# Kernel tuning notes

Measured on AMD Instinct MI355X. Metric: run time of the kernel, lower is better.

Reference implementation:

```python
import jax, jax.numpy as jnp
import numpy as np
from jax import lax

N_VAR, BATCH, N_IN, N_OUT, N_FEAT, T = 4, 32, 32, 32, 32, 256
EPS, COUPLING, GMAX, GMIN = 0.05, 0.2, 10.0, 0.01
DT, RMIN, RMAX, CMIN, CMAX = 0.1, 1e5, 1e7, 1e-7, 1e-4
ETA = np.array([0.05, 0.5, 0.3, 3.0], dtype=np.float32)  # printed-tanh activation params


def _init_theta(key, n_in, n_out):
    # xavier_uniform -> min-max normalize to [0,1], then bias-column construction as in pLayer.__init__
    a = float(np.sqrt(6.0 / (n_in + 2 + n_out)))
    t = jax.random.uniform(key, (n_in + 2, n_out), minval=-a, maxval=a)
    t = (t - t.min()) / (t.max() - t.min())
    t = t.at[-1, :].add(GMAX)
    t = t.at[-2, :].set(ETA[2] / (1.0 - ETA[2]) * (t[:-2].sum(0) + t[-1]))
    return t.astype(jnp.float32)


def setup_inputs():
    key = jax.random.key(0)
    kx, k1, k2 = jax.random.split(key, 3)
    x = jax.random.uniform(kx, (N_VAR, BATCH, N_IN, T), dtype=jnp.float32)
    theta1_ = _init_theta(k1, N_IN, N_OUT)
    theta2_ = _init_theta(k2, N_OUT * (N_FEAT + 1), N_OUT)
    # LearnableFilter init from beta_init (C_ fixed at -10, R_ is logit of normalized R)
    betas = np.linspace(0.1, 0.9, N_OUT)
    b0 = betas[:N_FEAT]
    b1 = betas[::-1][:N_FEAT]
    C_mean = 1.0 / (1.0 + np.exp(10.0)) * (CMAX - CMIN) + CMIN
    def r_(b):
        R_true = b * DT / (1.0 - b) / C_mean
        Rn = (R_true - RMIN) / (RMAX - RMIN)
        return np.log(Rn / (1.0 - Rn))
    Rlf_ = jnp.asarray(np.broadcast_to(np.stack([r_(b0), r_(b1)], -1), (N_OUT, N_FEAT, 2)).copy(), dtype=jnp.float32)
    Clf_ = jnp.full((N_OUT, N_FEAT, 2), -10.0, dtype=jnp.float32)
    return {"x": x, "theta1_": theta1_, "theta2_": theta2_, "Rlf_": Rlf_, "Clf_": Clf_}


def _theta_eff(theta_):
    # clamp + magnitude pruning with straight-through estimator
    t = jnp.clip(theta_, -GMAX, GMAX)
    t = jnp.where(jnp.abs(t) < GMIN, 0.0, t)
    return lax.stop_gradient(t) + theta_ - lax.stop_gradient(theta_)


def _pmac(a, theta_, key):
    # a: [N,B,Cin,T] -> [N,B,Cout,T]; printed MAC with sign-split weights and ideal inverter INV(a)=-a
    th = _theta_eff(theta_)
    noise = (jax.random.uniform(key, (N_VAR,) + th.shape) * 2.0 - 1.0) * EPS + 1.0
    thn = th[None] * noise  # [N,M,O]
    W = jnp.abs(thn) / (jnp.sum(jnp.abs(thn), axis=1, keepdims=True) + 1e-10)
    pos = (thn >= 0).astype(a.dtype)
    neg = 1.0 - pos
    ar = jnp.swapaxes(a, 2, 3)  # [N,B,T,Cin]
    ones = jnp.ones(ar.shape[:-1] + (1,), a.dtype)
    a_ext = jnp.concatenate([ar, ones, jnp.zeros_like(ones)], axis=-1)  # [N,B,T,M]
    a_neg = (-a_ext).at[..., -1].set(0.0)  # INV(a_ext) with last column zeroed
    z = jnp.einsum('nbtm,nmo->nbto', a_ext, W * pos) + jnp.einsum('nbtm,nmo->nbto', a_neg, W * neg)
    act = ETA[0] + ETA[1] * jnp.tanh((z - ETA[2]) * ETA[3])
    return jnp.swapaxes(act, 2, 3)


def _filter_bank(x, R_, C_, key):
    # x: [K,N,B,T]; first-order leaky integrator with fresh per-step R/C/mu noise, random init state
    K, N, B, Tt = x.shape
    Rt = jax.nn.sigmoid(R_) * (RMAX - RMIN) + RMIN  # [K]
    Ct = jax.nn.sigmoid(C_) * (CMAX - CMIN) + CMIN
    kR, kC, kmu, k0 = jax.random.split(key, 4)
    nR = (jax.random.uniform(kR, (Tt, K, N, 1)) * 2.0 - 1.0) * EPS + 1.0
    nC = (jax.random.uniform(kC, (Tt, K, N, 1)) * 2.0 - 1.0) * EPS + 1.0
    mu = jax.random.uniform(kmu, (Tt, K, N, 1)) * COUPLING + 1.0
    RC = mu * (Rt[None, :, None, None] * nR) * (Ct[None, :, None, None] * nC)
    beta = RC / (RC + DT)  # [T,K,N,1]
    s0 = jax.random.uniform(k0, (K, N, B))  # random_state=True
    xs = jnp.moveaxis(x, 3, 0)  # [T,K,N,B]
    def step(s, inp):
        x_t, b_t = inp
        return b_t * s + (1.0 - b_t) * x_t, s  # emit pre-update state (torch keeps init, drops last)
    _, outs = lax.scan(step, s0, (xs, beta))
    return jnp.moveaxis(outs, 0, 3)  # [K,N,B,T]


def reference(x, theta1_, theta2_, Rlf_, Clf_):
    key = jax.random.key(42)
    k1, k2, k3, k4 = jax.random.split(key, 4)
    a1 = _pmac(x, theta1_, k1)  # [N,B,C,T]
    N, B, C, Tt = a1.shape
    F = N_FEAT
    K = C * F
    xc = jnp.transpose(a1, (2, 0, 1, 3))  # [C,N,B,T]
    xk = jnp.broadcast_to(xc[:, None], (C, F, N, B, Tt)).reshape(K, N, B, Tt)
    y = _filter_bank(xk, Rlf_[..., 0].reshape(K), Clf_[..., 0].reshape(K), k2)
    y = _filter_bank(y, Rlf_[..., 1].reshape(K), Clf_[..., 1].reshape(K), k3)
    y = y.reshape(C, F, N, B, Tt)
    feats = jnp.concatenate([xc[:, None], y], axis=1)  # [C,F+1,N,B,T]
    h = jnp.transpose(feats, (2, 3, 0, 1, 4)).reshape(N, B, C * (F + 1), Tt)
    return _pmac(h, theta2_, k4)  # [N,B,N_out,T]
```

## Files before the change

### kernel.cpp

```cpp
#include <hip/hip_runtime.h>
#include <stdint.h>

#define C_RMIN 100000.0f
#define C_RMAX 10000000.0f
#define C_CMIN 1e-07f
#define C_CMAX 1e-04f
#define C_DT   0.1f
#define C_EPS  0.05f
#define C_COUP 0.2f

typedef __attribute__((ext_vector_type(8))) short bf16x8;
typedef __attribute__((ext_vector_type(4))) float floatx4;

__host__ __device__ inline void tf2x32(uint32_t k0, uint32_t k1,
                                       uint32_t& x0, uint32_t& x1) {
  uint32_t ks2 = k0 ^ k1 ^ 0x1BD11BDAu;
  uint32_t a = x0 + k0, b = x1 + k1;
#define TFR(r) a += b; b = (b << (r)) | (b >> (32 - (r))); b ^= a;
  TFR(13) TFR(15) TFR(26) TFR(6)
  a += k1;  b += ks2 + 1u;
  TFR(17) TFR(29) TFR(16) TFR(24)
  a += ks2; b += k0 + 2u;
  TFR(13) TFR(15) TFR(26) TFR(6)
  a += k0;  b += k1 + 3u;
  TFR(17) TFR(29) TFR(16) TFR(24)
  a += k1;  b += ks2 + 4u;
  TFR(13) TFR(15) TFR(26) TFR(6)
  a += ks2; b += k0 + 5u;
#undef TFR
  x0 = a; x1 = b;
}

__device__ inline float unif01(uint32_t k0, uint32_t k1, uint32_t e) {
  uint32_t x0 = 0u, x1 = e;
  tf2x32(k0, k1, x0, x1);
  uint32_t bits = x0 ^ x1;
  return __uint_as_float((bits >> 9) | 0x3F800000u) - 1.0f;
}

__device__ inline float theta_eff(float t) {
  t = fminf(fmaxf(t, -10.0f), 10.0f);
  return (fabsf(t) < 0.01f) ? 0.0f : t;
}

__device__ inline float sigmoidf(float x) { return 1.0f / (1.0f + expf(-x)); }

__device__ inline float noise_mul(float u) { return (u * 2.0f - 1.0f) * C_EPS + 1.0f; }

__global__ __launch_bounds__(256) void prep0_kernel(
    const float* __restrict__ Rlf, const float* __restrict__ Clf,
    const float* __restrict__ theta1, const float* __restrict__ theta2,
    float* __restrict__ beta12, float* __restrict__ S1eff,
    float* __restrict__ denom2p,
    uint32_t k1a, uint32_t k1b, uint32_t k4a, uint32_t k4b,
    uint32_t kR1a, uint32_t kR1b, uint32_t kC1a, uint32_t kC1b,
    uint32_t kM1a, uint32_t kM1b,
    uint32_t kR2a, uint32_t kR2b, uint32_t kC2a, uint32_t kC2b,
    uint32_t kM2a, uint32_t kM2b) {
  int bid = blockIdx.x;
  if (bid < 32) {
    int n = bid >> 3, p = bid & 7;
    int o = threadIdx.x & 31;
    int jc = threadIdx.x >> 5;
    int j0 = p * 8 + jc;
    float part = 0.0f;
    for (int j = j0; j < 1058; j += 64) {
      float t = theta_eff(theta2[j * 32 + o]);
      float u = unif01(k4a, k4b, (uint32_t)((n * 1058 + j) * 32 + o));
      part += fabsf(t * noise_mul(u));
    }
    __shared__ float red[256];
    red[jc * 32 + o] = part;
    __syncthreads();
    if (jc == 0) {
      float s = 0.0f;
      for (int q = 0; q < 8; ++q) s += red[q * 32 + o];
      denom2p[(n * 8 + p) * 32 + o] = s;
    }
  } else if (bid < 36) {
    int n = bid - 32;
    int o = threadIdx.x;
    if (o < 32) {
      float tn[34];
      float den = 0.0f;
      for (int m = 0; m < 34; ++m) {
        float t = theta_eff(theta1[m * 32 + o]);
        float u = unif01(k1a, k1b, (uint32_t)((n * 34 + m) * 32 + o));
        float v = t * noise_mul(u);
        tn[m] = v;
        den += fabsf(v);
      }
      den += 1e-10f;
      for (int m = 0; m < 33; ++m)
        S1eff[(n * 33 + m) * 32 + o] = tn[m] / den;
    }
  } else {
    int u = (bid - 36) * 256 + threadIdx.x;
    int k = u & 1023;
    int tc = (u >> 10) & 31;
    int n = u >> 15;
    float Rt1 = sigmoidf(Rlf[k * 2 + 0]) * (C_RMAX - C_RMIN) + C_RMIN;
    float Ct1 = sigmoidf(Clf[k * 2 + 0]) * (C_CMAX - C_CMIN) + C_CMIN;
    float Rt2 = sigmoidf(Rlf[k * 2 + 1]) * (C_RMAX - C_RMIN) + C_RMIN;
    float Ct2 = sigmoidf(Clf[k * 2 + 1]) * (C_CMAX - C_CMIN) + C_CMIN;
#pragma unroll
    for (int it = 0; it < 8; ++it) {
      int t = tc * 8 + it;
      uint32_t e = (uint32_t)((t * 1024 + k) * 4 + n);
      float nR1 = noise_mul(unif01(kR1a, kR1b, e));
      float nC1 = noise_mul(unif01(kC1a, kC1b, e));
      float mu1 = unif01(kM1a, kM1b, e) * C_COUP + 1.0f;
      float rc1 = mu1 * (Rt1 * nR1) * (Ct1 * nC1);
      float nR2 = noise_mul(unif01(kR2a, kR2b, e));
      float nC2 = noise_mul(unif01(kC2a, kC2b, e));
      float mu2 = unif01(kM2a, kM2b, e) * C_COUP + 1.0f;
      float rc2 = mu2 * (Rt2 * nR2) * (Ct2 * nC2);
      float2 bb = { rc1 / (rc1 + C_DT), rc2 / (rc2 + C_DT) };
      *(float2*)&beta12[(size_t)(((n * 256 + t) * 1024) + k) * 2] = bb;
    }
  }
}

__global__ __launch_bounds__(256) void prep1_kernel(
    const float* __restrict__ theta2, const float* __restrict__ denom2p,
    float* __restrict__ S2eff,
    const float* __restrict__ x, const float* __restrict__ S1eff,
    float* __restrict__ a1, uint32_t k4a, uint32_t k4b) {
  int bid = blockIdx.x;
  __shared__ float xs[32][256];
  if (bid < 128) {
    int n = bid >> 5, b = bid & 31;
    int t = threadIdx.x;
    const float* xp = x + (size_t)((n * 32 + b) * 32) * 256;
    for (int m = 0; m < 32; ++m) xs[m][t] = xp[m * 256 + t];
    __syncthreads();
    const float* S = S1eff + n * 33 * 32;
    float* ap = a1 + (size_t)((n * 32 + b) * 32) * 256;
    for (int o = 0; o < 32; ++o) {
      float z = S[32 * 32 + o];
#pragma unroll
      for (int m = 0; m < 32; ++m) z += xs[m][t] * S[m * 32 + o];
      ap[o * 256 + t] = 0.05f + 0.5f * tanhf((z - 0.3f) * 3.0f);
    }
  } else {
    int idx = (bid - 128) * 256 + threadIdx.x;
    if (idx >= 4 * 1057 * 32) return;
    int o = idx & 31;
    int r = idx >> 5;
    int j = r % 1057;
    int n = r / 1057;
    float den = 1e-10f;
#pragma unroll
    for (int p = 0; p < 8; ++p) den += denom2p[(n * 8 + p) * 32 + o];
    float t = theta_eff(theta2[j * 32 + o]);
    float u = unif01(k4a, k4b, (uint32_t)((n * 1058 + j) * 32 + o));
    S2eff[idx] = t * noise_mul(u) / den;
  }
}

#define YP 264
#define YPLANE (16 * YP)

__global__ __launch_bounds__(320) void fk5_kernel(
    const float* __restrict__ a1, const float* __restrict__ S2eff,
    const float* __restrict__ beta12, float* __restrict__ zpart,
    uint32_t k01a, uint32_t k01b, uint32_t k02a, uint32_t k02b) {
  int bid = blockIdx.x;
  int qr = bid & 3;
  int nb = bid >> 2;
  int n = nb >> 5, b = nb & 31;
  int tid = threadIdx.x;

  __shared__ __align__(16) uint8_t smem[50176];
  uint16_t* yh = (uint16_t*)smem;
  uint16_t* yl = (uint16_t*)(smem + 16896);
  short*    wf = (short*)(smem + 33792);

  const float* S2n = S2eff + (size_t)n * 1057 * 32;
  const float* a1nb = a1 + (size_t)nb * 8192;
  const float* bp = beta12 + ((size_t)n * 262144 + qr * 256) * 2;
  float* zout = zpart + (size_t)bid * 8192;

  float s1 = 0.0f, s2 = 0.0f;
  int cc = 0;

  if (tid < 256) {
    int k = qr * 256 + tid;
    uint32_t e0 = (uint32_t)((k * 4 + n) * 32 + b);
    s1 = unif01(k01a, k01b, e0);
    s2 = unif01(k02a, k02b, e0);
    cc = k >> 5;
    for (int it = 0; it < 32; ++it) {
      int widx = it * 256 + tid;
      int j = widx & 7;
      int lane_ = (widx >> 3) & 63;
      int ot = (widx >> 9) & 1;
      int ks = widx >> 10;
      int sub = ((lane_ >> 4) << 3) + j;
      int jrow = (qr * 8 + ks) * 33 + 1 + sub;
      float w = S2n[jrow * 32 + ot * 16 + (lane_ & 15)];
      uint32_t wb = __float_as_uint(w);
      uint32_t hi = (wb + 0x7FFFu + ((wb >> 16) & 1u)) >> 16;
      wf[(ks * 2 + ot) * 512 + lane_ * 8 + j] = (short)(uint16_t)hi;
    }
  }
  __syncthreads();

  for (int c = 0; c <= 16; ++c) {
    if (tid < 256) {
      if (c < 16) {
        uint16_t* yhb = yh + (c & 1) * YPLANE;
        uint16_t* ylb = yl + (c & 1) * YPLANE;
        int t0 = c * 16;
#pragma unroll
        for (int it = 0; it < 16; ++it) {
          int t = t0 + it;
          uint32_t sb = __float_as_uint(s2);
          uint32_t hi = sb >> 16;
          float fhi = __uint_as_float(sb & 0xFFFF0000u);
          uint32_t lo = __float_as_uint(s2 - fhi) >> 16;
          yhb[it * YP + tid] = (uint16_t)hi;
          ylb[it * YP + tid] = (uint16_t)lo;
          float2 bb = *(const float2*)&bp[(size_t)(t * 1024 + tid) * 2];
          float xv = a1nb[cc * 256 + t];
          s2 = bb.y * s2 + (1.0f - bb.y) * s1;
          s1 = bb.x * s1 + (1.0f - bb.x) * xv;
        }
      }
    } else if (c >= 1) {
      int lane = tid - 256;
      int tc = lane & 15, q = lane >> 4;
      const uint16_t* yhr = yh + ((c - 1) & 1) * YPLANE + tc * YP + q * 8;
      const uint16_t* ylr = yl + ((c - 1) & 1) * YPLANE + tc * YP + q * 8;
      floatx4 acc0a = {0,0,0,0}, acc0b = {0,0,0,0};
      floatx4 acc1a = {0,0,0,0}, acc1b = {0,0,0,0};
#pragma unroll
      for (int ks = 0; ks < 8; ++ks) {
        bf16x8 ah = *(const bf16x8*)(yhr + ks * 32);
        bf16x8 al = *(const bf16x8*)(ylr + ks * 32);
        bf16x8 bh0 = *(const bf16x8*)&wf[(ks * 2 + 0) * 512 + lane * 8];
        bf16x8 bh1 = *(const bf16x8*)&wf[(ks * 2 + 1) * 512 + lane * 8];
        if (ks & 1) {
          acc0b = __builtin_amdgcn_mfma_f32_16x16x32_bf16(ah, bh0, acc0b, 0, 0, 0);
          acc0b = __builtin_amdgcn_mfma_f32_16x16x32_bf16(al, bh0, acc0b, 0, 0, 0);
          acc1b = __builtin_amdgcn_mfma_f32_16x16x32_bf16(ah, bh1, acc1b, 0, 0, 0);
          acc1b = __builtin_amdgcn_mfma_f32_16x16x32_bf16(al, bh1, acc1b, 0, 0, 0);
        } else {
          acc0a = __builtin_amdgcn_mfma_f32_16x16x32_bf16(ah, bh0, acc0a, 0, 0, 0);
          acc0a = __builtin_amdgcn_mfma_f32_16x16x32_bf16(al, bh0, acc0a, 0, 0, 0);
          acc1a = __builtin_amdgcn_mfma_f32_16x16x32_bf16(ah, bh1, acc1a, 0, 0, 0);
          acc1a = __builtin_amdgcn_mfma_f32_16x16x32_bf16(al, bh1, acc1a, 0, 0, 0);
        }
      }
      int t0 = (c - 1) * 16;
      floatx4 r0 = acc0a + acc0b;
      floatx4 r1 = acc1a + acc1b;
      *(floatx4*)&zout[tc * 256 + t0 + q * 4] = r0;
      *(floatx4*)&zout[(16 + tc) * 256 + t0 + q * 4] = r1;
    }
    __syncthreads();
  }
}

__global__ __launch_bounds__(256) void cb_kernel(
    const float* __restrict__ a1, const float* __restrict__ S2eff,
    const float* __restrict__ zpart, float* __restrict__ out) {
  int nb = blockIdx.x;
  int n = nb >> 5;
  int t = threadIdx.x;
  __shared__ float xs[32][256];
  const float* a1nb = a1 + (size_t)nb * 8192;
  for (int c = 0; c < 32; ++c) xs[c][t] = a1nb[c * 256 + t];
  __syncthreads();
  const float* S2n = S2eff + (size_t)n * 1057 * 32;
  const float* zp = zpart + (size_t)nb * 4 * 8192;
  float* op = out + (size_t)nb * 8192;
  for (int o = 0; o < 32; ++o) {
    float z = S2n[1056 * 32 + o];
#pragma unroll
    for (int c = 0; c < 32; ++c) z += xs[c][t] * S2n[(c * 33) * 32 + o];
    z += zp[o * 256 + t] + zp[8192 + o * 256 + t] +
         zp[16384 + o * 256 + t] + zp[24576 + o * 256 + t];
    op[o * 256 + t] = 0.05f + 0.5f * tanhf((z - 0.3f) * 3.0f);
  }
}

struct KeyPair { uint32_t a, b; };

static inline void split4_host(KeyPair key, KeyPair out[4]) {
  for (uint32_t i = 0; i < 4; ++i) {
    uint32_t x0 = 0u, x1 = i;
    tf2x32(key.a, key.b, x0, x1);
    out[i] = {x0, x1};
  }
}

extern "C" void kernel_launch(void* const* d_in, const int* in_sizes, int n_in,
                              void* d_out, int out_size, void* d_ws, size_t ws_size,
                              hipStream_t stream) {
  const float* x   = (const float*)d_in[0];
  const float* th1 = (const float*)d_in[1];
  const float* th2 = (const float*)d_in[2];
  const float* Rlf = (const float*)d_in[3];
  const float* Clf = (const float*)d_in[4];
  float* out = (float*)d_out;
  float* ws = (float*)d_ws;

  float* S1     = ws;
  float* den2p  = ws + 4224;
  float* S2     = ws + 5248;
  float* a1     = ws + 140544;
  float* beta12 = ws + 1189120;
  float* zpart  = ws + 3286272;

  KeyPair root{0u, 42u};
  KeyPair kk[4];  split4_host(root, kk);
  KeyPair f1[4];  split4_host(kk[1], f1);
  KeyPair f2[4];  split4_host(kk[2], f2);

  prep0_kernel<<<dim3(548), dim3(256), 0, stream>>>(
      Rlf, Clf, th1, th2, beta12, S1, den2p,
      kk[0].a, kk[0].b, kk[3].a, kk[3].b,
      f1[0].a, f1[0].b, f1[1].a, f1[1].b, f1[2].a, f1[2].b,
      f2[0].a, f2[0].b, f2[1].a, f2[1].b, f2[2].a, f2[2].b);
  prep1_kernel<<<dim3(657), dim3(256), 0, stream>>>(
      th2, den2p, S2, x, S1, a1, kk[3].a, kk[3].b);
  fk5_kernel<<<dim3(512), dim3(320), 0, stream>>>(
      a1, S2, beta12, zpart, f1[3].a, f1[3].b, f2[3].a, f2[3].b);
  cb_kernel<<<dim3(128), dim3(256), 0, stream>>>(a1, S2, zpart, out);
}
```

Before: 158.7 us.

## Fuse prep kernels and compute second-layer weights on the fly in consumers

Removes the separate prep1 kernel by computing the first-layer weights inside each layer-1 MAC block and generating the second-layer normalized noisy weights directly in fk6 and cb2 from theta2 and the partial denominators. This drops one kernel launch and the S1/S2 global round trips. In exchange, the threefry noise and the layer-1 normalization are recomputed redundantly per block, and the layer-1 MAC now competes with beta generation inside one kernel.

Result: faster. 142.8 us (-10.1%).

```diff
diff --git a/kernel.cpp b/kernel.cpp
--- a/kernel.cpp
+++ b/kernel.cpp
@@ -47,21 +47,27 @@
 
 __device__ inline float noise_mul(float u) { return (u * 2.0f - 1.0f) * C_EPS + 1.0f; }
 
-__global__ __launch_bounds__(256) void prep0_kernel(
+__global__ __launch_bounds__(256) void prep_kernel(
     const float* __restrict__ Rlf, const float* __restrict__ Clf,
     const float* __restrict__ theta1, const float* __restrict__ theta2,
-    float* __restrict__ beta12, float* __restrict__ S1eff,
+    const float* __restrict__ x,
+    float* __restrict__ beta12, float* __restrict__ a1,
     float* __restrict__ denom2p,
     uint32_t k1a, uint32_t k1b, uint32_t k4a, uint32_t k4b,
     uint32_t kR1a, uint32_t kR1b, uint32_t kC1a, uint32_t kC1b,
     uint32_t kM1a, uint32_t kM1b,
     uint32_t kR2a, uint32_t kR2b, uint32_t kC2a, uint32_t kC2b,
     uint32_t kM2a, uint32_t kM2b) {
+  __shared__ float red[256];
+  __shared__ float vsm[34 * 32];
+  __shared__ float S1s[33 * 32];
+  __shared__ float xs[32][256];
   int bid = blockIdx.x;
+  int tid = threadIdx.x;
   if (bid < 32) {
     int n = bid >> 3, p = bid & 7;
-    int o = threadIdx.x & 31;
-    int jc = threadIdx.x >> 5;
+    int o = tid & 31;
+    int jc = tid >> 5;
     int j0 = p * 8 + jc;
     float part = 0.0f;
     for (int j = j0; j < 1058; j += 64) {
@@ -69,7 +75,6 @@
       float u = unif01(k4a, k4b, (uint32_t)((n * 1058 + j) * 32 + o));
       part += fabsf(t * noise_mul(u));
     }
-    __shared__ float red[256];
     red[jc * 32 + o] = part;
     __syncthreads();
     if (jc == 0) {
@@ -77,25 +82,39 @@
       for (int q = 0; q < 8; ++q) s += red[q * 32 + o];
       denom2p[(n * 8 + p) * 32 + o] = s;
     }
-  } else if (bid < 36) {
-    int n = bid - 32;
-    int o = threadIdx.x;
-    if (o < 32) {
-      float tn[34];
-      float den = 0.0f;
-      for (int m = 0; m < 34; ++m) {
-        float t = theta_eff(theta1[m * 32 + o]);
-        float u = unif01(k1a, k1b, (uint32_t)((n * 34 + m) * 32 + o));
-        float v = t * noise_mul(u);
-        tn[m] = v;
-        den += fabsf(v);
-      }
-      den += 1e-10f;
-      for (int m = 0; m < 33; ++m)
-        S1eff[(n * 33 + m) * 32 + o] = tn[m] / den;
+  } else if (bid < 160) {
+    int blk = bid - 32;
+    int n = blk >> 5, b = blk & 31;
+    int o = tid & 31, mq = tid >> 5;
+    float dp = 0.0f;
+    for (int m = mq; m < 34; m += 8) {
+      float t = theta_eff(theta1[m * 32 + o]);
+      float v = t * noise_mul(unif01(k1a, k1b, (uint32_t)((n * 34 + m) * 32 + o)));
+      vsm[m * 32 + o] = v;
+      dp += fabsf(v);
+    }
+    red[mq * 32 + o] = dp;
+    const float* xp = x + (size_t)((n * 32 + b) * 32) * 256;
+    __syncthreads();
+    for (int idx = tid; idx < 33 * 32; idx += 256) {
+      int oo = idx & 31;
+      float den = 1e-10f;
+#pragma unroll
+      for (int q = 0; q < 8; ++q) den += red[q * 32 + oo];
+      S1s[idx] = vsm[idx] / den;
+    }
+    for (int m = 0; m < 32; ++m) xs[m][tid] = xp[m * 256 + tid];
+    __syncthreads();
+    float* ap = a1 + (size_t)((n * 32 + b) * 32) * 256;
+    int t = tid;
+    for (int oo = 0; oo < 32; ++oo) {
+      float z = S1s[32 * 32 + oo];
+#pragma unroll
+      for (int m = 0; m < 32; ++m) z += xs[m][t] * S1s[m * 32 + oo];
+      ap[oo * 256 + t] = 0.05f + 0.5f * tanhf((z - 0.3f) * 3.0f);
     }
   } else {
-    int u = (bid - 36) * 256 + threadIdx.x;
+    int u = (bid - 160) * 256 + tid;
     int k = u & 1023;
     int tc = (u >> 10) & 31;
     int n = u >> 15;
@@ -121,50 +140,15 @@
   }
 }
 
-__global__ __launch_bounds__(256) void prep1_kernel(
-    const float* __restrict__ theta2, const float* __restrict__ denom2p,
-    float* __restrict__ S2eff,
-    const float* __restrict__ x, const float* __restrict__ S1eff,
-    float* __restrict__ a1, uint32_t k4a, uint32_t k4b) {
-  int bid = blockIdx.x;
-  __shared__ float xs[32][256];
-  if (bid < 128) {
-    int n = bid >> 5, b = bid & 31;
-    int t = threadIdx.x;
-    const float* xp = x + (size_t)((n * 32 + b) * 32) * 256;
-    for (int m = 0; m < 32; ++m) xs[m][t] = xp[m * 256 + t];
-    __syncthreads();
-    const float* S = S1eff + n * 33 * 32;
-    float* ap = a1 + (size_t)((n * 32 + b) * 32) * 256;
-    for (int o = 0; o < 32; ++o) {
-      float z = S[32 * 32 + o];
-#pragma unroll
-      for (int m = 0; m < 32; ++m) z += xs[m][t] * S[m * 32 + o];
-      ap[o * 256 + t] = 0.05f + 0.5f * tanhf((z - 0.3f) * 3.0f);
-    }
-  } else {
-    int idx = (bid - 128) * 256 + threadIdx.x;
-    if (idx >= 4 * 1057 * 32) return;
-    int o = idx & 31;
-    int r = idx >> 5;
-    int j = r % 1057;
-    int n = r / 1057;
-    float den = 1e-10f;
-#pragma unroll
-    for (int p = 0; p < 8; ++p) den += denom2p[(n * 8 + p) * 32 + o];
-    float t = theta_eff(theta2[j * 32 + o]);
-    float u = unif01(k4a, k4b, (uint32_t)((n * 1058 + j) * 32 + o));
-    S2eff[idx] = t * noise_mul(u) / den;
-  }
-}
-
 #define YP 264
 #define YPLANE (16 * YP)
 
-__global__ __launch_bounds__(320) void fk5_kernel(
-    const float* __restrict__ a1, const float* __restrict__ S2eff,
+__global__ __launch_bounds__(320) void fk6_kernel(
+    const float* __restrict__ a1, const float* __restrict__ theta2,
+    const float* __restrict__ denom2p,
     const float* __restrict__ beta12, float* __restrict__ zpart,
-    uint32_t k01a, uint32_t k01b, uint32_t k02a, uint32_t k02b) {
+    uint32_t k01a, uint32_t k01b, uint32_t k02a, uint32_t k02b,
+    uint32_t k4a, uint32_t k4b) {
   int bid = blockIdx.x;
   int qr = bid & 3;
   int nb = bid >> 2;
@@ -175,11 +159,19 @@
   uint16_t* yh = (uint16_t*)smem;
   uint16_t* yl = (uint16_t*)(smem + 16896);
   short*    wf = (short*)(smem + 33792);
-
-  const float* S2n = S2eff + (size_t)n * 1057 * 32;
+  __shared__ float sden[32];
+
   const float* a1nb = a1 + (size_t)nb * 8192;
   const float* bp = beta12 + ((size_t)n * 262144 + qr * 256) * 2;
   float* zout = zpart + (size_t)bid * 8192;
+
+  if (tid < 32) {
+    float d = 1e-10f;
+#pragma unroll
+    for (int q = 0; q < 8; ++q) d += denom2p[(n * 8 + q) * 32 + tid];
+    sden[tid] = d;
+  }
+  __syncthreads();
 
   float s1 = 0.0f, s2 = 0.0f;
   int cc = 0;
@@ -198,7 +190,10 @@
       int ks = widx >> 10;
       int sub = ((lane_ >> 4) << 3) + j;
       int jrow = (qr * 8 + ks) * 33 + 1 + sub;
-      float w = S2n[jrow * 32 + ot * 16 + (lane_ & 15)];
+      int oo = ot * 16 + (lane_ & 15);
+      float th = theta_eff(theta2[jrow * 32 + oo]);
+      float u = unif01(k4a, k4b, (uint32_t)((n * 1058 + jrow) * 32 + oo));
+      float w = th * noise_mul(u) / sden[oo];
       uint32_t wb = __float_as_uint(w);
       uint32_t hi = (wb + 0x7FFFu + ((wb >> 16) & 1u)) >> 16;
       wf[(ks * 2 + ot) * 512 + lane_ * 8 + j] = (short)(uint16_t)hi;
@@ -262,23 +257,40 @@
   }
 }
 
-__global__ __launch_bounds__(256) void cb_kernel(
-    const float* __restrict__ a1, const float* __restrict__ S2eff,
-    const float* __restrict__ zpart, float* __restrict__ out) {
+__global__ __launch_bounds__(256) void cb2_kernel(
+    const float* __restrict__ a1, const float* __restrict__ theta2,
+    const float* __restrict__ denom2p,
+    const float* __restrict__ zpart, float* __restrict__ out,
+    uint32_t k4a, uint32_t k4b) {
   int nb = blockIdx.x;
   int n = nb >> 5;
   int t = threadIdx.x;
   __shared__ float xs[32][256];
+  __shared__ float wd[33 * 32];
+  __shared__ float sden[32];
+  if (t < 32) {
+    float d = 1e-10f;
+#pragma unroll
+    for (int q = 0; q < 8; ++q) d += denom2p[(n * 8 + q) * 32 + t];
+    sden[t] = d;
+  }
   const float* a1nb = a1 + (size_t)nb * 8192;
   for (int c = 0; c < 32; ++c) xs[c][t] = a1nb[c * 256 + t];
   __syncthreads();
-  const float* S2n = S2eff + (size_t)n * 1057 * 32;
+  for (int idx = t; idx < 33 * 32; idx += 256) {
+    int r = idx >> 5, oo = idx & 31;
+    int j = (r < 32) ? r * 33 : 1056;
+    float th = theta_eff(theta2[j * 32 + oo]);
+    float u = unif01(k4a, k4b, (uint32_t)((n * 1058 + j) * 32 + oo));
+    wd[idx] = th * noise_mul(u) / sden[oo];
+  }
+  __syncthreads();
   const float* zp = zpart + (size_t)nb * 4 * 8192;
   float* op = out + (size_t)nb * 8192;
   for (int o = 0; o < 32; ++o) {
-    float z = S2n[1056 * 32 + o];
-#pragma unroll
-    for (int c = 0; c < 32; ++c) z += xs[c][t] * S2n[(c * 33) * 32 + o];
+    float z = wd[32 * 32 + o];
+#pragma unroll
+    for (int c = 0; c < 32; ++c) z += xs[c][t] * wd[c * 32 + o];
     z += zp[o * 256 + t] + zp[8192 + o * 256 + t] +
          zp[16384 + o * 256 + t] + zp[24576 + o * 256 + t];
     op[o * 256 + t] = 0.05f + 0.5f * tanhf((z - 0.3f) * 3.0f);
@@ -306,26 +318,24 @@
   float* out = (float*)d_out;
   float* ws = (float*)d_ws;
 
-  float* S1     = ws;
-  float* den2p  = ws + 4224;
-  float* S2     = ws + 5248;
-  float* a1     = ws + 140544;
-  float* beta12 = ws + 1189120;
-  float* zpart  = ws + 3286272;
+  float* den2p  = ws;
+  float* a1     = ws + 1024;
+  float* beta12 = ws + 1049600;
+  float* zpart  = ws + 3146752;
 
   KeyPair root{0u, 42u};
   KeyPair kk[4];  split4_host(root, kk);
   KeyPair f1[4];  split4_host(kk[1], f1);
   KeyPair f2[4];  split4_host(kk[2], f2);
 
-  prep0_kernel<<<dim3(548), dim3(256), 0, stream>>>(
-      Rlf, Clf, th1, th2, beta12, S1, den2p,
+  prep_kernel<<<dim3(672), dim3(256), 0, stream>>>(
+      Rlf, Clf, th1, th2, x, beta12, a1, den2p,
       kk[0].a, kk[0].b, kk[3].a, kk[3].b,
       f1[0].a, f1[0].b, f1[1].a, f1[1].b, f1[2].a, f1[2].b,
       f2[0].a, f2[0].b, f2[1].a, f2[1].b, f2[2].a, f2[2].b);
-  prep1_kernel<<<dim3(657), dim3(256), 0, stream>>>(
-      th2, den2p, S2, x, S1, a1, kk[3].a, kk[3].b);
-  fk5_kernel<<<dim3(512), dim3(320), 0, stream>>>(
-      a1, S2, beta12, zpart, f1[3].a, f1[3].b, f2[3].a, f2[3].b);
-  cb_kernel<<<dim3(128), dim3(256), 0, stream>>>(a1, S2, zpart, out);
-}
+  fk6_kernel<<<dim3(512), dim3(320), 0, stream>>>(
+      a1, th2, den2p, beta12, zpart,
+      f1[3].a, f1[3].b, f2[3].a, f2[3].b, kk[3].a, kk[3].b);
+  cb2_kernel<<<dim3(128), dim3(256), 0, stream>>>(
+      a1, th2, den2p, zpart, out, kk[3].a, kk[3].b);
+}
```
